# Kernel tuning notes

Hardware: AMD Instinct MI355X
Metric: run time of the kernel (lower is better)

The kernel has to match this reference:

```python
import jax, jax.numpy as jnp
import numpy as np

AVGF = 30   # number of averaged temporal segments (timesteps of the TTM)
TK = 10     # hardcoded number of transformer 'layers' in the source
HA = 1      # hardcoded number of heads


def _ln(v, g, b, eps=1e-5):
    # LayerNorm over the last (only) dim of a 1-D vector
    mu = jnp.mean(v)
    var = jnp.mean((v - mu) ** 2)
    return (v - mu) / jnp.sqrt(var + eps) * g + b


def setup_inputs() -> dict:
    key = jax.random.key(0)
    ks = jax.random.split(key, 8)
    C, S, T = 32, 32, 360
    M = C * S  # 1024 = M_size1
    sc = 0.02  # scale randn params for numerical sanity (source uses raw randn)
    x = jax.random.normal(ks[0], (C, S, T), jnp.float32)
    weight = jax.random.normal(ks[1], (M, M), jnp.float32) * sc
    Wq = jax.random.normal(ks[2], (TK, HA, M // HA, M), jnp.float32) * sc
    Wk = jax.random.normal(ks[3], (TK, HA, M // HA, M), jnp.float32) * sc
    Wv = jax.random.normal(ks[4], (TK, HA, M // HA, M), jnp.float32) * sc
    Wo = jax.random.normal(ks[5], (TK, M, M), jnp.float32) * sc
    ln_g = jnp.ones((M,), jnp.float32); ln_b = jnp.zeros((M,), jnp.float32)
    lnz_g = jnp.ones((M,), jnp.float32); lnz_b = jnp.zeros((M,), jnp.float32)
    fc1_w = jax.random.normal(ks[6], (4 * M, M), jnp.float32) * sc
    fc1_b = jnp.zeros((4 * M,), jnp.float32)
    fc2_w = jax.random.normal(ks[7], (M, 4 * M), jnp.float32) * sc
    fc2_b = jnp.zeros((M,), jnp.float32)
    return dict(x=x, weight=weight, Wq=Wq, Wk=Wk, Wv=Wv, Wo=Wo,
                ln_g=ln_g, ln_b=ln_b, lnz_g=lnz_g, lnz_b=lnz_b,
                fc1_w=fc1_w, fc1_b=fc1_b, fc2_w=fc2_w, fc2_b=fc2_b)


def reference(x, weight, Wq, Wk, Wv, Wo, ln_g, ln_b, lnz_g, lnz_b,
              fc1_w, fc1_b, fc2_w, fc2_b):
    C, S, T = x.shape
    M = C * S
    seg = T // AVGF
    Dh = M // HA
    # redefine(): transpose(0,2) then segment-average over the temporal dim, flatten
    xcf = jnp.transpose(x, (2, 1, 0)).reshape(AVGF, seg, S * C).mean(axis=1)  # (AVGF, M)
    # sinusoidal positional 'bias' exactly as the source loop builds it
    i = jnp.arange(AVGF, dtype=jnp.float32)[:, None]
    j = jnp.arange(0, M, 2, dtype=jnp.float32)[None, :]
    ang = i / jnp.power(jnp.float32(10000.0), 2.0 * j / M)
    pe = jnp.zeros((AVGF, M), jnp.float32).at[:, 0::2].set(jnp.sin(ang)).at[:, 1::2].set(jnp.cos(ang))
    s0 = xcf @ weight.T + pe  # savespace init: weight @ x[i] + bias
    scale = 1.0 / jnp.sqrt(jnp.float32(Dh))

    def step(vcum, s):
        # vcum[a]: sum over previously processed timesteps of r*v at layer a
        for a in range(TK):
            z = _ln(s, ln_g, ln_b)
            q = jnp.einsum('hdm,m->hd', Wq[a], z)  # (HA, Dh)
            k = jnp.einsum('hdm,m->hd', Wk[a], z)
            v = jnp.einsum('hdm,m->hd', Wv[a], z)
            score = jnp.sum(q * scale * k, axis=-1)          # (HA,) scalar per head
            r = jax.nn.softmax(score[:, None], axis=-1)[:, 0]  # softmax of a scalar == 1
            rv = r[:, None] * v
            s = Wo[a] @ vcum[a].reshape(-1) + s              # imv = sum over subj < i
            s = _ln(s, lnz_g, lnz_b) + s
            s = fc2_w @ jax.nn.gelu(fc1_w @ s + fc1_b, approximate=False) + fc2_b
            vcum = vcum.at[a].add(rv)                        # current timestep now visible to future
        return vcum, s

    vcum0 = jnp.zeros((TK, HA, Dh), jnp.float32)
    _, out = jax.lax.scan(step, vcum0, s0)  # sequential over timesteps
    return out.reshape(AVGF, S, C)
```

## Files before the change

### kernel.cpp

```cpp
#include <hip/hip_runtime.h>

#define MDIM 1024
#define H4   4096
#define TKL  10
#define NT   30
#define NWFR 39
#define GBLK 256
#define GTHR 1024
#define AGENT __HIP_MEMORY_SCOPE_AGENT

typedef _Float16 h2v __attribute__((ext_vector_type(2)));
typedef unsigned int uv4 __attribute__((ext_vector_type(4)));
typedef float fv4 __attribute__((ext_vector_type(4)));
union U16 { uv4 u; h2v h[4]; _Float16 f[8]; };

__device__ __forceinline__ float wred(float v) {
#pragma unroll
  for (int o = 32; o; o >>= 1) v += __shfl_xor(v, o, 64);
  return v;
}

__device__ __forceinline__ float dot16(const U16& w, const U16& x, float acc) {
  acc = __builtin_amdgcn_fdot2(w.h[0], x.h[0], acc, false);
  acc = __builtin_amdgcn_fdot2(w.h[1], x.h[1], acc, false);
  acc = __builtin_amdgcn_fdot2(w.h[2], x.h[2], acc, false);
  acc = __builtin_amdgcn_fdot2(w.h[3], x.h[3], acc, false);
  return acc;
}

__device__ __forceinline__ void stg16(const void* p, uv4 v) {
  asm volatile("global_store_dwordx4 %0, %1, off sc0 sc1" :: "v"(p), "v"(v) : "memory");
}

__global__ void k_cvt(const float* __restrict__ in, _Float16* __restrict__ out, int n8) {
  int g = blockIdx.x * blockDim.x + threadIdx.x;
  if (g >= n8) return;
  const float4* p = (const float4*)in;
  float4 a = p[2 * g], b = p[2 * g + 1];
  U16 o;
  o.f[0] = (_Float16)a.x; o.f[1] = (_Float16)a.y;
  o.f[2] = (_Float16)a.z; o.f[3] = (_Float16)a.w;
  o.f[4] = (_Float16)b.x; o.f[5] = (_Float16)b.y;
  o.f[6] = (_Float16)b.z; o.f[7] = (_Float16)b.w;
  ((uv4*)out)[g] = o.u;
}

__global__ void k_xcf(const float* __restrict__ x, float* __restrict__ xcf) {
  int idx = blockIdx.x * blockDim.x + threadIdx.x;
  if (idx >= NT * MDIM) return;
  int i = idx >> 10, m = idx & (MDIM - 1);
  int c = m & 31, s = m >> 5;
  const float* p = x + c * (32 * 360) + s * 360 + i * 12;
  float acc = 0.f;
#pragma unroll
  for (int k = 0; k < 12; ++k) acc += p[k];
  xcf[idx] = acc * (1.0f / 12.0f);
}

__global__ void k_s0(const float* __restrict__ xcf, const float* __restrict__ W,
                     float* __restrict__ S, float* __restrict__ Smir) {
  int wid = (blockIdx.x * blockDim.x + threadIdx.x) >> 6;
  int lane = threadIdx.x & 63;
  if (wid >= NT * MDIM) return;
  int i = wid >> 10, m = wid & (MDIM - 1);
  const float4* wr = (const float4*)(W + (size_t)m * MDIM);
  const float4* xr = (const float4*)(xcf + i * MDIM);
  float acc = 0.f;
#pragma unroll
  for (int k = 0; k < 4; ++k) {
    float4 w = wr[lane + (k << 6)];
    float4 xv = xr[lane + (k << 6)];
    acc += w.x * xv.x + w.y * xv.y + w.z * xv.z + w.w * xv.w;
  }
  acc = wred(acc);
  if (lane == 0) {
    int e = m & ~1;
    float ang = (float)i / powf(10000.0f, (float)e / 512.0f);
    float pe = (m & 1) ? cosf(ang) : sinf(ang);
    float val = acc + pe;
    S[wid] = val;
    Smir[((size_t)i * NT + i) * MDIM + m] = val;
  }
}

__device__ __forceinline__ void gbar(unsigned* bar, unsigned ep) {
  asm volatile("s_waitcnt vmcnt(0)" ::: "memory");
  __syncthreads();
  if (threadIdx.x == 0) {
    unsigned* leaf = bar + ((blockIdx.x & 7) << 5);
    const unsigned prev = __hip_atomic_fetch_add(leaf, 1u, __ATOMIC_RELAXED, AGENT);
    if (prev == ep * 32u - 1u) {
      const unsigned r = __hip_atomic_fetch_add(bar + 256, 1u, __ATOMIC_RELAXED, AGENT);
      if (r == ep * 8u - 1u)
        __hip_atomic_store(bar + 288, ep, __ATOMIC_RELAXED, AGENT);
    }
    while (__hip_atomic_load(bar + 288, __ATOMIC_RELAXED, AGENT) < ep)
      __builtin_amdgcn_s_sleep(2);
  }
  __syncthreads();
}

__global__ __launch_bounds__(GTHR) void k_main(
    const _Float16* __restrict__ Wvh, const _Float16* __restrict__ Woh,
    const _Float16* __restrict__ fc1h, const float* __restrict__ fc1b,
    const _Float16* __restrict__ fc2h, const float* __restrict__ fc2b,
    const float* __restrict__ lng, const float* __restrict__ lnb,
    const float* __restrict__ lzg, const float* __restrict__ lzb,
    float* __restrict__ S, float* __restrict__ ocum,
    float* __restrict__ Smir, float* __restrict__ Omir, float* __restrict__ vmir,
    _Float16* __restrict__ hmir, unsigned* __restrict__ bar) {
  __shared__ __align__(16) _Float16 fc1L[16 * MDIM];
  __shared__ __align__(16) _Float16 WoL[3 * 16 * MDIM];
  __shared__ __align__(16) _Float16 x2L[TKL * MDIM];
  __shared__ __align__(16) _Float16 zvL[3 * MDIM];
  __shared__ __align__(16) float4 stats[TKL];
  __shared__ __align__(16) float vgs[3][16];
  __shared__ __align__(16) _Float16 hgelL2[TKL][16];
  __shared__ float part[4][4][TKL];
  __shared__ __align__(16) float sOut[TKL][4];
  _Float16* hL = x2L;

  const int tid = threadIdx.x;
  const int lane = tid & 63;
  const int bwave = tid >> 6;
  const int b = blockIdx.x;
  unsigned ep = 0;

  __builtin_amdgcn_fence(__ATOMIC_ACQUIRE, "agent");

  int aR[3], rgR[3];
  bool okR[3];
#pragma unroll
  for (int r = 0; r < 3; ++r) {
    const int g = b + (r << 8);
    okR[r] = g < 640;
    aR[r] = g >> 6;
    rgR[r] = g & 63;
  }
  {
    const _Float16* s1 = fc1h + (size_t)b * 16384;
#pragma unroll
    for (int r = 0; r < 2; ++r) {
      const int s = tid + (r << 10);
      *(uv4*)(fc1L + (s << 3)) = *(const uv4*)(s1 + (s << 3));
    }
#pragma unroll
    for (int r = 0; r < 3; ++r)
      if (okR[r]) {
        const _Float16* src = Woh + ((size_t)aR[r] << 20) + ((size_t)rgR[r] << 14);
#pragma unroll
        for (int it = 0; it < 2; ++it) {
          const int s = tid + (it << 10);
          *(uv4*)(WoL + r * 16384 + (s << 3)) = *(const uv4*)(src + (s << 3));
        }
      }
  }
  __syncthreads();

  for (int t = 0; t < NWFR; ++t) {
    const int alo = (t - (NT - 1)) > 0 ? (t - (NT - 1)) : 0;
    const int ahi = t < (TKL - 1) ? t : (TKL - 1);
    const int nc = ahi - alo + 1;
    const float* Smirt = Smir + (size_t)t * NT * MDIM;
    const float* Omirt = Omir + (size_t)t * TKL * MDIM;
    bool actR[3];
    int cz[3];
#pragma unroll
    for (int r = 0; r < 3; ++r) {
      actR[r] = okR[r] && aR[r] >= alo && aR[r] <= ahi && (t - aR[r]) != NT - 1;
      cz[r] = actR[r] ? (aR[r] - alo) : -1;
    }

    if (bwave < nc) {
      const int a = alo + bwave, i = t - a;
      const fv4* sp = (const fv4*)(Smirt + (size_t)i * MDIM + (lane << 4));
      const fv4* op = (const fv4*)(Omirt + (size_t)a * MDIM + (lane << 4));
      fv4 sv[4], tv[4];
#pragma unroll
      for (int k = 0; k < 4; ++k) { sv[k] = sp[k]; tv[k] = sv[k] + op[k]; }
      float s1 = 0.f, t1 = 0.f;
#pragma unroll
      for (int k = 0; k < 4; ++k)
#pragma unroll
        for (int e = 0; e < 4; ++e) { s1 += sv[k][e]; t1 += tv[k][e]; }
      const float mu_s = wred(s1) * (1.0f / MDIM);
      const float mu_t = wred(t1) * (1.0f / MDIM);
      float s2 = 0.f, t2 = 0.f;
#pragma unroll
      for (int k = 0; k < 4; ++k)
#pragma unroll
        for (int e = 0; e < 4; ++e) {
          float d = sv[k][e] - mu_s; s2 += d * d;
          float f = tv[k][e] - mu_t; t2 += f * f;
        }
      const float var_s = wred(s2) * (1.0f / MDIM);
      const float var_t = wred(t2) * (1.0f / MDIM);
      if (!lane)
        stats[bwave] = make_float4(mu_s, rsqrtf(var_s + 1e-5f),
                                   mu_t, rsqrtf(var_t + 1e-5f));
    }
    __syncthreads();

#pragma unroll
    for (int p = 0; p < 2; ++p) {
      const int c = (p << 3) + (tid >> 7);
      if (c < nc) {
        const int a = alo + c, i = t - a;
        const int e = (tid & 127) << 3;
        const float4 st4 = stats[c];
        fv4 sA = *(const fv4*)(Smirt + (size_t)i * MDIM + e);
        fv4 sB = *(const fv4*)(Smirt + (size_t)i * MDIM + e + 4);
        fv4 oA = *(const fv4*)(Omirt + (size_t)a * MDIM + e);
        fv4 oB = *(const fv4*)(Omirt + (size_t)a * MDIM + e + 4);
        fv4 g1A = *(const fv4*)(lng + e), g1B = *(const fv4*)(lng + e + 4);
        fv4 b1A = *(const fv4*)(lnb + e), b1B = *(const fv4*)(lnb + e + 4);
        fv4 g2A = *(const fv4*)(lzg + e), g2B = *(const fv4*)(lzg + e + 4);
        fv4 b2A = *(const fv4*)(lzb + e), b2B = *(const fv4*)(lzb + e + 4);
        U16 zz, xx;
#pragma unroll
        for (int k = 0; k < 4; ++k) {
          zz.f[k] = (_Float16)((sA[k] - st4.x) * st4.y * g1A[k] + b1A[k]);
          zz.f[4 + k] = (_Float16)((sB[k] - st4.x) * st4.y * g1B[k] + b1B[k]);
          const float u0 = sA[k] + oA[k], u1 = sB[k] + oB[k];
          xx.f[k] = (_Float16)((u0 - st4.z) * st4.w * g2A[k] + b2A[k] + u0);
          xx.f[4 + k] = (_Float16)((u1 - st4.z) * st4.w * g2B[k] + b2B[k] + u1);
        }
        *(uv4*)(x2L + c * MDIM + e) = xx.u;
        if (c == cz[0]) *(uv4*)(zvL + e) = zz.u;
        if (c == cz[1]) *(uv4*)(zvL + MDIM + e) = zz.u;
        if (c == cz[2]) *(uv4*)(zvL + 2 * MDIM + e) = zz.u;
      }
    }
    __syncthreads();

#pragma unroll
    for (int r = 0; r < 3; ++r)
      if (actR[r]) {
        const _Float16* wp =
            Wvh + ((size_t)aR[r] << 20) + ((size_t)((rgR[r] << 4) | bwave) << 10);
        U16 w0, w1, z0, z1;
        w0.u = *(const uv4*)(wp + (lane << 3));
        w1.u = *(const uv4*)(wp + 512 + (lane << 3));
        z0.u = *(const uv4*)(zvL + r * MDIM + (lane << 3));
        z1.u = *(const uv4*)(zvL + r * MDIM + 512 + (lane << 3));
        float acc = dot16(w0, z0, 0.f);
        acc = dot16(w1, z1, acc);
        acc = wred(acc);
        if (!lane) vgs[r][bwave] = acc;
      }
    {
      U16 f0, f1;
      f0.u = *(const uv4*)(fc1L + bwave * MDIM + (lane << 3));
      f1.u = *(const uv4*)(fc1L + bwave * MDIM + 512 + (lane << 3));
      const float bias = fc1b[(b << 4) | bwave];
      float sel = 0.f;
#pragma unroll
      for (int c = 0; c < TKL; ++c)
        if (c < nc) {
          U16 x0, x1;
          x0.u = *(const uv4*)(x2L + c * MDIM + (lane << 3));
          x1.u = *(const uv4*)(x2L + c * MDIM + 512 + (lane << 3));
          float acc = dot16(f0, x0, 0.f);
          acc = dot16(f1, x1, acc);
          acc = wred(acc);
          sel = (lane == c) ? acc : sel;
        }
      const float xg = sel + bias;
      const float ge = 0.5f * xg * (1.0f + erff(xg * 0.70710678118654752f));
      if (lane < nc) hgelL2[lane][bwave] = (_Float16)ge;
    }
    __syncthreads();
    if (bwave < nc && lane < 2) {
      uv4 hv = *(const uv4*)(&hgelL2[bwave][lane << 3]);
      stg16(hmir + ((size_t)t * TKL + alo + bwave) * H4 + (b << 4) + (lane << 3), hv);
    }
    if (bwave >= 13 && lane < 4) {
      const int r = bwave - 13;
      if (actR[r]) {
        fv4 vv = *(const fv4*)(&vgs[r][lane << 2]);
        stg16(vmir + ((size_t)t * TKL + aR[r]) * MDIM + (rgR[r] << 4) + (lane << 2),
              __builtin_bit_cast(uv4, vv));
      }
    }
    ++ep; gbar(bar, ep);

    const int rl = bwave >> 2, kq = bwave & 3;
    U16 w2a, w2b;
    {
      const _Float16* fp = fc2h + ((size_t)((b << 2) | rl) << 12) + (kq << 10);
      w2a.u = *(const uv4*)(fp + (lane << 3));
      w2b.u = *(const uv4*)(fp + 512 + (lane << 3));
    }
    {
      const int r = tid >> 8, e4 = (tid & 255) << 2;
      if (r < 3 && actR[r]) {
        fv4 v = *(const fv4*)(vmir + ((size_t)t * TKL + aR[r]) * MDIM + e4);
        zvL[r * MDIM + e4] = (_Float16)v[0];
        zvL[r * MDIM + e4 + 1] = (_Float16)v[1];
        zvL[r * MDIM + e4 + 2] = (_Float16)v[2];
        zvL[r * MDIM + e4 + 3] = (_Float16)v[3];
      }
      const int q = tid >> 9, idx = (tid & 511) << 3;
      if (q < nc)
        *(uv4*)(hL + q * H4 + idx) =
            *(const uv4*)(hmir + ((size_t)t * TKL + alo + q) * H4 + idx);
    }
    __syncthreads();
#pragma unroll
    for (int r = 0; r < 3; ++r)
      if (actR[r]) {
        U16 w0, w1, v0, v1;
        w0.u = *(const uv4*)(WoL + r * 16384 + bwave * MDIM + (lane << 3));
        w1.u = *(const uv4*)(WoL + r * 16384 + bwave * MDIM + 512 + (lane << 3));
        v0.u = *(const uv4*)(zvL + r * MDIM + (lane << 3));
        v1.u = *(const uv4*)(zvL + r * MDIM + 512 + (lane << 3));
        float acc = dot16(w0, v0, 0.f);
        acc = dot16(w1, v1, acc);
        acc = wred(acc);
        if (!lane) vgs[r][bwave] = acc;
      }
#pragma unroll
    for (int q = 0; q < 2; ++q)
      if (q < nc) {
        U16 h0, h1;
        h0.u = *(const uv4*)(hL + q * H4 + (kq << 10) + (lane << 3));
        h1.u = *(const uv4*)(hL + q * H4 + (kq << 10) + 512 + (lane << 3));
        float acc = dot16(w2a, h0, 0.f);
        acc = dot16(w2b, h1, acc);
        acc = wred(acc);
        if (!lane) part[rl][kq][q] = acc;
      }
    __syncthreads();
    if (bwave >= 13 && lane < 4) {
      const int r = bwave - 13;
      if (actR[r]) {
        const int R = (rgR[r] << 4) + (lane << 2);
        float* po = ocum + aR[r] * MDIM + R;
        fv4 old = *(const fv4*)po;
        fv4 nv = old + *(const fv4*)(&vgs[r][lane << 2]);
        *(fv4*)po = nv;
        stg16(Omir + ((size_t)(t + 1) * TKL + aR[r]) * MDIM + R,
              __builtin_bit_cast(uv4, nv));
      }
    }
    for (int ch = 1; ch < 5; ++ch) {
      const int c0 = ch << 1;
      if (c0 >= nc) break;
      {
        const int q = tid >> 9, idx = (tid & 511) << 3;
        const int c = c0 + q;
        if (c < nc)
          *(uv4*)(hL + q * H4 + idx) =
              *(const uv4*)(hmir + ((size_t)t * TKL + alo + c) * H4 + idx);
      }
      __syncthreads();
#pragma unroll
      for (int q = 0; q < 2; ++q) {
        const int c = c0 + q;
        if (c < nc) {
          U16 h0, h1;
          h0.u = *(const uv4*)(hL + q * H4 + (kq << 10) + (lane << 3));
          h1.u = *(const uv4*)(hL + q * H4 + (kq << 10) + 512 + (lane << 3));
          float acc = dot16(w2a, h0, 0.f);
          acc = dot16(w2b, h1, acc);
          acc = wred(acc);
          if (!lane) part[rl][kq][c] = acc;
        }
      }
      __syncthreads();
    }

    if (bwave < nc && lane < 4)
      sOut[bwave][lane] = part[lane][0][bwave] + part[lane][1][bwave] +
                          part[lane][2][bwave] + part[lane][3][bwave] +
                          fc2b[(b << 2) | lane];
    __syncthreads();
    if (bwave < nc && !lane) {
      const int a = alo + bwave, i = t - a;
      fv4 sv = *(const fv4*)(&sOut[bwave][0]);
      if (a == TKL - 1)
        *(fv4*)(S + (size_t)i * MDIM + (b << 2)) = sv;
      else
        stg16(Smir + ((size_t)(t + 1) * NT + i) * MDIM + (b << 2),
              __builtin_bit_cast(uv4, sv));
    }
    ++ep; gbar(bar, ep);
  }
}

extern "C" void kernel_launch(void* const* d_in, const int* in_sizes, int n_in,
                              void* d_out, int out_size, void* d_ws, size_t ws_size,
                              hipStream_t stream) {
  const float* x    = (const float*)d_in[0];
  const float* W    = (const float*)d_in[1];
  const float* Wv   = (const float*)d_in[4];
  const float* Wo   = (const float*)d_in[5];
  const float* lng  = (const float*)d_in[6];
  const float* lnb  = (const float*)d_in[7];
  const float* lzg  = (const float*)d_in[8];
  const float* lzb  = (const float*)d_in[9];
  const float* fc1w = (const float*)d_in[10];
  const float* fc1b = (const float*)d_in[11];
  const float* fc2w = (const float*)d_in[12];
  const float* fc2b = (const float*)d_in[13];
  float* S = (float*)d_out;

  float* xcf  = (float*)d_ws;
  float* ocum = xcf + 30720;
  unsigned* bar = (unsigned*)(ocum + 10240);
  float* Smir = (float*)(bar + 512);
  float* Omir = Smir + 1228800;
  float* vmir = Omir + 409600;
  _Float16* hmir = (_Float16*)(vmir + 409600);
  _Float16* Wvh  = hmir + 1638400;
  _Float16* Woh  = Wvh + 10485760;
  _Float16* fc1h = Woh + 10485760;
  _Float16* fc2h = fc1h + 4194304;

  hipLaunchKernelGGL(k_cvt, dim3(5120), dim3(256), 0, stream, Wv, Wvh, 1310720);
  hipLaunchKernelGGL(k_cvt, dim3(5120), dim3(256), 0, stream, Wo, Woh, 1310720);
  hipLaunchKernelGGL(k_cvt, dim3(2048), dim3(256), 0, stream, fc1w, fc1h, 524288);
  hipLaunchKernelGGL(k_cvt, dim3(2048), dim3(256), 0, stream, fc2w, fc2h, 524288);
  hipLaunchKernelGGL(k_xcf, dim3((NT * MDIM + 255) / 256), dim3(256), 0, stream, x, xcf);
  hipLaunchKernelGGL(k_s0, dim3(NT * MDIM / 4), dim3(256), 0, stream, xcf, W, S, Smir);
  hipMemsetAsync(ocum, 0, 10240 * sizeof(float), stream);
  hipMemsetAsync(Omir, 0, 409600 * sizeof(float), stream);
  hipMemsetAsync(bar, 0, 2048, stream);

  void* args[] = {(void*)&Wvh, (void*)&Woh, (void*)&fc1h, (void*)&fc1b,
                  (void*)&fc2h, (void*)&fc2b, (void*)&lng, (void*)&lnb,
                  (void*)&lzg, (void*)&lzb, (void*)&S,   (void*)&ocum,
                  (void*)&Smir, (void*)&Omir, (void*)&vmir, (void*)&hmir,
                  (void*)&bar};
  hipLaunchCooperativeKernel((void*)k_main, dim3(GBLK), dim3(GTHR), args, 0, stream);
}
```

Measured before the change: 1.020 ms.

## Double persistent grid to 512 blocks and stream Wo from global memory

Doubles the persistent cooperative grid from 256 to 512 blocks, halving each block's share of fc1/fc2 rows and Wv/Wo row groups. fc2 weights are now cached in LDS while Wo is read from global memory each step, to fit LDS limits and allow two blocks per CU. The barrier tree counts are adjusted and the cooperative launch is replaced with a normal launch. This spreads the per-step matvec work across more CUs but doubles barrier participants and relies on all 512 blocks being co-resident without a cooperative-launch guarantee.

```diff
diff --git a/kernel.cpp b/kernel.cpp
--- a/kernel.cpp
+++ b/kernel.cpp
@@ -5,12 +5,13 @@
 #define TKL  10
 #define NT   30
 #define NWFR 39
-#define GBLK 256
+#define GBLK 512
 #define GTHR 1024
 #define AGENT __HIP_MEMORY_SCOPE_AGENT
 
 typedef _Float16 h2v __attribute__((ext_vector_type(2)));
 typedef unsigned int uv4 __attribute__((ext_vector_type(4)));
+typedef unsigned int uv2 __attribute__((ext_vector_type(2)));
 typedef float fv4 __attribute__((ext_vector_type(4)));
 union U16 { uv4 u; h2v h[4]; _Float16 f[8]; };
 
@@ -30,6 +31,9 @@
 
 __device__ __forceinline__ void stg16(const void* p, uv4 v) {
   asm volatile("global_store_dwordx4 %0, %1, off sc0 sc1" :: "v"(p), "v"(v) : "memory");
+}
+__device__ __forceinline__ void stg8(const void* p, uv2 v) {
+  asm volatile("global_store_dwordx2 %0, %1, off sc0 sc1" :: "v"(p), "v"(v) : "memory");
 }
 
 __global__ void k_cvt(const float* __restrict__ in, _Float16* __restrict__ out, int n8) {
@@ -89,7 +93,7 @@
   if (threadIdx.x == 0) {
     unsigned* leaf = bar + ((blockIdx.x & 7) << 5);
     const unsigned prev = __hip_atomic_fetch_add(leaf, 1u, __ATOMIC_RELAXED, AGENT);
-    if (prev == ep * 32u - 1u) {
+    if (prev == ep * 64u - 1u) {
       const unsigned r = __hip_atomic_fetch_add(bar + 256, 1u, __ATOMIC_RELAXED, AGENT);
       if (r == ep * 8u - 1u)
         __hip_atomic_store(bar + 288, ep, __ATOMIC_RELAXED, AGENT);
@@ -100,7 +104,7 @@
   __syncthreads();
 }
 
-__global__ __launch_bounds__(GTHR) void k_main(
+__global__ __launch_bounds__(GTHR, 8) void k_main(
     const _Float16* __restrict__ Wvh, const _Float16* __restrict__ Woh,
     const _Float16* __restrict__ fc1h, const float* __restrict__ fc1b,
     const _Float16* __restrict__ fc2h, const float* __restrict__ fc2b,
@@ -109,15 +113,15 @@
     float* __restrict__ S, float* __restrict__ ocum,
     float* __restrict__ Smir, float* __restrict__ Omir, float* __restrict__ vmir,
     _Float16* __restrict__ hmir, unsigned* __restrict__ bar) {
-  __shared__ __align__(16) _Float16 fc1L[16 * MDIM];
-  __shared__ __align__(16) _Float16 WoL[3 * 16 * MDIM];
+  __shared__ __align__(16) _Float16 fc1L[8 * MDIM];
+  __shared__ __align__(16) _Float16 fc2L[2 * H4];
   __shared__ __align__(16) _Float16 x2L[TKL * MDIM];
-  __shared__ __align__(16) _Float16 zvL[3 * MDIM];
+  __shared__ __align__(16) _Float16 zvL[2 * MDIM];
   __shared__ __align__(16) float4 stats[TKL];
-  __shared__ __align__(16) float vgs[3][16];
-  __shared__ __align__(16) _Float16 hgelL2[TKL][16];
-  __shared__ float part[4][4][TKL];
-  __shared__ __align__(16) float sOut[TKL][4];
+  __shared__ __align__(16) float vgs[2][16];
+  __shared__ __align__(16) _Float16 hgelL2[TKL][8];
+  __shared__ float part[2][8][TKL];
+  __shared__ float sOut[TKL][2];
   _Float16* hL = x2L;
 
   const int tid = threadIdx.x;
@@ -128,33 +132,17 @@
 
   __builtin_amdgcn_fence(__ATOMIC_ACQUIRE, "agent");
 
-  int aR[3], rgR[3];
-  bool okR[3];
-#pragma unroll
-  for (int r = 0; r < 3; ++r) {
-    const int g = b + (r << 8);
+  int aR[2], rgR[2];
+  bool okR[2];
+#pragma unroll
+  for (int r = 0; r < 2; ++r) {
+    const int g = b + (r << 9);
     okR[r] = g < 640;
     aR[r] = g >> 6;
     rgR[r] = g & 63;
   }
-  {
-    const _Float16* s1 = fc1h + (size_t)b * 16384;
-#pragma unroll
-    for (int r = 0; r < 2; ++r) {
-      const int s = tid + (r << 10);
-      *(uv4*)(fc1L + (s << 3)) = *(const uv4*)(s1 + (s << 3));
-    }
-#pragma unroll
-    for (int r = 0; r < 3; ++r)
-      if (okR[r]) {
-        const _Float16* src = Woh + ((size_t)aR[r] << 20) + ((size_t)rgR[r] << 14);
-#pragma unroll
-        for (int it = 0; it < 2; ++it) {
-          const int s = tid + (it << 10);
-          *(uv4*)(WoL + r * 16384 + (s << 3)) = *(const uv4*)(src + (s << 3));
-        }
-      }
-  }
+  *(uv4*)(fc1L + (tid << 3)) = *(const uv4*)(fc1h + (size_t)b * 8192 + (tid << 3));
+  *(uv4*)(fc2L + (tid << 3)) = *(const uv4*)(fc2h + (size_t)b * 8192 + (tid << 3));
   __syncthreads();
 
   for (int t = 0; t < NWFR; ++t) {
@@ -163,10 +151,10 @@
     const int nc = ahi - alo + 1;
     const float* Smirt = Smir + (size_t)t * NT * MDIM;
     const float* Omirt = Omir + (size_t)t * TKL * MDIM;
-    bool actR[3];
-    int cz[3];
-#pragma unroll
-    for (int r = 0; r < 3; ++r) {
+    bool actR[2];
+    int cz[2];
+#pragma unroll
+    for (int r = 0; r < 2; ++r) {
       actR[r] = okR[r] && aR[r] >= alo && aR[r] <= ahi && (t - aR[r]) != NT - 1;
       cz[r] = actR[r] ? (aR[r] - alo) : -1;
     }
@@ -228,34 +216,36 @@
         *(uv4*)(x2L + c * MDIM + e) = xx.u;
         if (c == cz[0]) *(uv4*)(zvL + e) = zz.u;
         if (c == cz[1]) *(uv4*)(zvL + MDIM + e) = zz.u;
-        if (c == cz[2]) *(uv4*)(zvL + 2 * MDIM + e) = zz.u;
-      }
-    }
-    __syncthreads();
-
-#pragma unroll
-    for (int r = 0; r < 3; ++r)
+      }
+    }
+    __syncthreads();
+
+#pragma unroll
+    for (int r = 0; r < 2; ++r)
       if (actR[r]) {
         const _Float16* wp =
             Wvh + ((size_t)aR[r] << 20) + ((size_t)((rgR[r] << 4) | bwave) << 10);
         U16 w0, w1, z0, z1;
         w0.u = *(const uv4*)(wp + (lane << 3));
         w1.u = *(const uv4*)(wp + 512 + (lane << 3));
-        z0.u = *(const uv4*)(zvL + r * MDIM + (lane << 3));
-        z1.u = *(const uv4*)(zvL + r * MDIM + 512 + (lane << 3));
+        z0.u = *(const uv4*)(zvL + (r << 10) + (lane << 3));
+        z1.u = *(const uv4*)(zvL + (r << 10) + 512 + (lane << 3));
         float acc = dot16(w0, z0, 0.f);
         acc = dot16(w1, z1, acc);
         acc = wred(acc);
         if (!lane) vgs[r][bwave] = acc;
       }
     {
+      const int rw = bwave & 7;
+      const int base = (bwave >> 3) * 5;
       U16 f0, f1;
-      f0.u = *(const uv4*)(fc1L + bwave * MDIM + (lane << 3));
-      f1.u = *(const uv4*)(fc1L + bwave * MDIM + 512 + (lane << 3));
-      const float bias = fc1b[(b << 4) | bwave];
+      f0.u = *(const uv4*)(fc1L + rw * MDIM + (lane << 3));
+      f1.u = *(const uv4*)(fc1L + rw * MDIM + 512 + (lane << 3));
+      const float bias = fc1b[(b << 3) | rw];
       float sel = 0.f;
 #pragma unroll
-      for (int c = 0; c < TKL; ++c)
+      for (int cc = 0; cc < 5; ++cc) {
+        const int c = base + cc;
         if (c < nc) {
           U16 x0, x1;
           x0.u = *(const uv4*)(x2L + c * MDIM + (lane << 3));
@@ -263,19 +253,20 @@
           float acc = dot16(f0, x0, 0.f);
           acc = dot16(f1, x1, acc);
           acc = wred(acc);
-          sel = (lane == c) ? acc : sel;
+          sel = (lane == cc) ? acc : sel;
         }
+      }
       const float xg = sel + bias;
       const float ge = 0.5f * xg * (1.0f + erff(xg * 0.70710678118654752f));
-      if (lane < nc) hgelL2[lane][bwave] = (_Float16)ge;
-    }
-    __syncthreads();
-    if (bwave < nc && lane < 2) {
-      uv4 hv = *(const uv4*)(&hgelL2[bwave][lane << 3]);
-      stg16(hmir + ((size_t)t * TKL + alo + bwave) * H4 + (b << 4) + (lane << 3), hv);
-    }
-    if (bwave >= 13 && lane < 4) {
-      const int r = bwave - 13;
+      if (lane < 5 && base + lane < nc) hgelL2[base + lane][rw] = (_Float16)ge;
+    }
+    __syncthreads();
+    if (bwave < nc && lane == 0) {
+      uv4 hv = *(const uv4*)(&hgelL2[bwave][0]);
+      stg16(hmir + ((size_t)t * TKL + alo + bwave) * H4 + (b << 3), hv);
+    }
+    if (bwave >= 14 && lane < 4) {
+      const int r = bwave - 14;
       if (actR[r]) {
         fv4 vv = *(const fv4*)(&vgs[r][lane << 2]);
         stg16(vmir + ((size_t)t * TKL + aR[r]) * MDIM + (rgR[r] << 4) + (lane << 2),
@@ -284,22 +275,12 @@
     }
     ++ep; gbar(bar, ep);
 
-    const int rl = bwave >> 2, kq = bwave & 3;
-    U16 w2a, w2b;
+#pragma unroll
+    for (int r = 0; r < 2; ++r)
+      if (actR[r])
+        zvL[(r << 10) + tid] =
+            (_Float16)vmir[((size_t)t * TKL + aR[r]) * MDIM + tid];
     {
-      const _Float16* fp = fc2h + ((size_t)((b << 2) | rl) << 12) + (kq << 10);
-      w2a.u = *(const uv4*)(fp + (lane << 3));
-      w2b.u = *(const uv4*)(fp + 512 + (lane << 3));
-    }
-    {
-      const int r = tid >> 8, e4 = (tid & 255) << 2;
-      if (r < 3 && actR[r]) {
-        fv4 v = *(const fv4*)(vmir + ((size_t)t * TKL + aR[r]) * MDIM + e4);
-        zvL[r * MDIM + e4] = (_Float16)v[0];
-        zvL[r * MDIM + e4 + 1] = (_Float16)v[1];
-        zvL[r * MDIM + e4 + 2] = (_Float16)v[2];
-        zvL[r * MDIM + e4 + 3] = (_Float16)v[3];
-      }
       const int q = tid >> 9, idx = (tid & 511) << 3;
       if (q < nc)
         *(uv4*)(hL + q * H4 + idx) =
@@ -307,32 +288,35 @@
     }
     __syncthreads();
 #pragma unroll
-    for (int r = 0; r < 3; ++r)
+    for (int r = 0; r < 2; ++r)
       if (actR[r]) {
+        const _Float16* wp =
+            Woh + ((size_t)aR[r] << 20) + ((size_t)((rgR[r] << 4) | bwave) << 10);
         U16 w0, w1, v0, v1;
-        w0.u = *(const uv4*)(WoL + r * 16384 + bwave * MDIM + (lane << 3));
-        w1.u = *(const uv4*)(WoL + r * 16384 + bwave * MDIM + 512 + (lane << 3));
-        v0.u = *(const uv4*)(zvL + r * MDIM + (lane << 3));
-        v1.u = *(const uv4*)(zvL + r * MDIM + 512 + (lane << 3));
+        w0.u = *(const uv4*)(wp + (lane << 3));
+        w1.u = *(const uv4*)(wp + 512 + (lane << 3));
+        v0.u = *(const uv4*)(zvL + (r << 10) + (lane << 3));
+        v1.u = *(const uv4*)(zvL + (r << 10) + 512 + (lane << 3));
         float acc = dot16(w0, v0, 0.f);
         acc = dot16(w1, v1, acc);
         acc = wred(acc);
         if (!lane) vgs[r][bwave] = acc;
       }
+    const int rl = bwave >> 3, kq = bwave & 7;
+    U16 w2;
+    w2.u = *(const uv4*)(fc2L + (rl << 12) + (kq << 9) + (lane << 3));
 #pragma unroll
     for (int q = 0; q < 2; ++q)
       if (q < nc) {
-        U16 h0, h1;
-        h0.u = *(const uv4*)(hL + q * H4 + (kq << 10) + (lane << 3));
-        h1.u = *(const uv4*)(hL + q * H4 + (kq << 10) + 512 + (lane << 3));
-        float acc = dot16(w2a, h0, 0.f);
-        acc = dot16(w2b, h1, acc);
+        U16 h0;
+        h0.u = *(const uv4*)(hL + q * H4 + (kq << 9) + (lane << 3));
+        float acc = dot16(w2, h0, 0.f);
         acc = wred(acc);
         if (!lane) part[rl][kq][q] = acc;
       }
     __syncthreads();
-    if (bwave >= 13 && lane < 4) {
-      const int r = bwave - 13;
+    if (bwave >= 14 && lane < 4) {
+      const int r = bwave - 14;
       if (actR[r]) {
         const int R = (rgR[r] << 4) + (lane << 2);
         float* po = ocum + aR[r] * MDIM + R;
@@ -358,11 +342,9 @@
       for (int q = 0; q < 2; ++q) {
         const int c = c0 + q;
         if (c < nc) {
-          U16 h0, h1;
-          h0.u = *(const uv4*)(hL + q * H4 + (kq << 10) + (lane << 3));
-          h1.u = *(const uv4*)(hL + q * H4 + (kq << 10) + 512 + (lane << 3));
-          float acc = dot16(w2a, h0, 0.f);
-          acc = dot16(w2b, h1, acc);
+          U16 h0;
+          h0.u = *(const uv4*)(hL + q * H4 + (kq << 9) + (lane << 3));
+          float acc = dot16(w2, h0, 0.f);
           acc = wred(acc);
           if (!lane) part[rl][kq][c] = acc;
         }
@@ -370,19 +352,24 @@
       __syncthreads();
     }
 
-    if (bwave < nc && lane < 4)
-      sOut[bwave][lane] = part[lane][0][bwave] + part[lane][1][bwave] +
-                          part[lane][2][bwave] + part[lane][3][bwave] +
-                          fc2b[(b << 2) | lane];
+    if (bwave < nc && lane < 2) {
+      float s = fc2b[(b << 1) | lane];
+#pragma unroll
+      for (int k = 0; k < 8; ++k) s += part[lane][k][bwave];
+      sOut[bwave][lane] = s;
+    }
     __syncthreads();
     if (bwave < nc && !lane) {
       const int a = alo + bwave, i = t - a;
-      fv4 sv = *(const fv4*)(&sOut[bwave][0]);
-      if (a == TKL - 1)
-        *(fv4*)(S + (size_t)i * MDIM + (b << 2)) = sv;
-      else
-        stg16(Smir + ((size_t)(t + 1) * NT + i) * MDIM + (b << 2),
-              __builtin_bit_cast(uv4, sv));
+      const float v0 = sOut[bwave][0], v1 = sOut[bwave][1];
+      if (a == TKL - 1) {
+        *(float2*)(S + (size_t)i * MDIM + (b << 1)) = make_float2(v0, v1);
+      } else {
+        uv2 sv2;
+        sv2.x = __float_as_uint(v0);
+        sv2.y = __float_as_uint(v1);
+        stg8(Smir + ((size_t)(t + 1) * NT + i) * MDIM + (b << 1), sv2);
+      }
     }
     ++ep; gbar(bar, ep);
   }
@@ -427,10 +414,7 @@
   hipMemsetAsync(Omir, 0, 409600 * sizeof(float), stream);
   hipMemsetAsync(bar, 0, 2048, stream);
 
-  void* args[] = {(void*)&Wvh, (void*)&Woh, (void*)&fc1h, (void*)&fc1b,
-                  (void*)&fc2h, (void*)&fc2b, (void*)&lng, (void*)&lnb,
-                  (void*)&lzg, (void*)&lzb, (void*)&S,   (void*)&ocum,
-                  (void*)&Smir, (void*)&Omir, (void*)&vmir, (void*)&hmir,
-                  (void*)&bar};
-  hipLaunchCooperativeKernel((void*)k_main, dim3(GBLK), dim3(GTHR), args, 0, stream);
-}
+  hipLaunchKernelGGL(k_main, dim3(GBLK), dim3(GTHR), 0, stream,
+                     Wvh, Woh, fc1h, fc1b, fc2h, fc2b, lng, lnb, lzg, lzb,
+                     S, ocum, Smir, Omir, vmir, hmir, bar);
+}
```

Result: slower. 1.595 ms (+56.4%).
